# Kernel tuning notes

Measured on AMD Instinct MI355X. Metric: run time of the kernel, lower is better.

## Reference

```python
import jax, jax.numpy as jnp
import numpy as np
from jax import lax

B, T, D, H, L = 64, 1024, 256, 1024, 2


def setup_inputs() -> dict:
    key = jax.random.key(0)
    ks = jax.random.split(key, 9)
    s = 0.03  # small init so tanh/sigmoid stay in sane range
    return {
        "x": jax.random.normal(ks[0], (B, T, D), dtype=jnp.float32),
        "W_ih0": jax.random.normal(ks[1], (4 * H, D), dtype=jnp.float32) * s,
        "W_hh0": jax.random.normal(ks[2], (4 * H, H), dtype=jnp.float32) * s,
        "b_ih0": jax.random.normal(ks[3], (4 * H,), dtype=jnp.float32) * s,
        "b_hh0": jax.random.normal(ks[4], (4 * H,), dtype=jnp.float32) * s,
        "W_ih1": jax.random.normal(ks[5], (4 * H, H), dtype=jnp.float32) * s,
        "W_hh1": jax.random.normal(ks[6], (4 * H, H), dtype=jnp.float32) * s,
        "b_ih1": jax.random.normal(ks[7], (4 * H,), dtype=jnp.float32) * s,
        "b_hh1": jax.random.normal(ks[8], (4 * H,), dtype=jnp.float32) * s,
    }


def _lstm_layer(x, W_ih, W_hh, b_ih, b_hh):
    """Single LSTM layer over full sequence. x: [B,T,Din]. Returns (ys [B,T,H], h [B,H], c [B,H])."""
    b, t = x.shape[0], x.shape[1]
    h_dim = W_hh.shape[1]
    # Precompute input projections for all timesteps in one GEMM.
    xg = jnp.einsum('bti,gi->btg', x, W_ih) + b_ih + b_hh  # [B,T,4H]

    def step(carry, xg_t):
        h, c = carry
        g = xg_t + h @ W_hh.T  # [B,4H]
        i, f, gg, o = jnp.split(g, 4, axis=-1)  # PyTorch gate order i,f,g,o
        i = jax.nn.sigmoid(i)
        f = jax.nn.sigmoid(f)
        gg = jnp.tanh(gg)
        o = jax.nn.sigmoid(o)
        c = f * c + i * gg
        h = o * jnp.tanh(c)
        return (h, c), h

    h0 = jnp.zeros((b, h_dim), x.dtype)
    (h, c), ys = lax.scan(step, (h0, h0), jnp.swapaxes(xg, 0, 1))
    return jnp.swapaxes(ys, 0, 1), h, c


def reference(x, W_ih0, W_hh0, b_ih0, b_hh0, W_ih1, W_hh1, b_ih1, b_hh1):
    # Dropout layers are identity in eval mode; nn.LSTM inter-layer dropout
    # is also inactive in eval, so the math is a plain stacked LSTM whose
    # final (h, c) per layer is returned, matching the torch forward().
    y0, h0_, c0_ = _lstm_layer(x, W_ih0, W_hh0, b_ih0, b_hh0)
    _, h1_, c1_ = _lstm_layer(y0, W_ih1, W_hh1, b_ih1, b_hh1)
    h = jnp.stack([h0_, h1_], axis=0)  # [L,B,H]
    c = jnp.stack([c0_, c1_], axis=0)  # [L,B,H]
    return (h, c)
```

## Files before the change

kernel.cpp:

```cpp
#include <hip/hip_runtime.h>

#define NWG     256
#define TPB     256
#define NL0     128
#define T_STEPS 1024
#define HD      1024
#define DIN     256
#define K0      1280
#define K1      2048
#define K0P     1288
#define K1P     2056
#define SMEM_BYTES (32*K1P*2)

#define HSLAB_BYTES 131072ull
#define HSLAB_U64   16384
#define HIST_DEPTH  1025
#define HIST_BYTES  (HIST_DEPTH*HSLAB_BYTES)
#define X8_BYTES    33554432ull
#define FLAGS_BYTES 32768ull

typedef float  f32x4  __attribute__((ext_vector_type(4)));
typedef __bf16 bf16x8 __attribute__((ext_vector_type(8)));
typedef int    i32x4  __attribute__((ext_vector_type(4)));
typedef unsigned long long u64;

__device__ __forceinline__ unsigned short f2bf(float f){
  union { float f; unsigned u; } a; a.f = f;
  unsigned u = a.u;
  u += 0x7fffu + ((u >> 16) & 1u);
  return (unsigned short)(u >> 16);
}
__device__ __forceinline__ float sigmf(float x){ return 1.0f/(1.0f + __expf(-x)); }
__device__ __forceinline__ float tanhf_fast(float x){ return 2.0f*sigmf(2.0f*x) - 1.0f; }

__device__ __forceinline__ u64 ld64c(const u64* p){
  return __hip_atomic_load(p, __ATOMIC_RELAXED, __HIP_MEMORY_SCOPE_AGENT);
}
__device__ __forceinline__ unsigned ldflag(const unsigned* p){
  return __hip_atomic_load(p, __ATOMIC_RELAXED, __HIP_MEMORY_SCOPE_AGENT);
}
__device__ __forceinline__ void stflag(unsigned* p, unsigned v){
  __hip_atomic_store(p, v, __ATOMIC_RELAXED, __HIP_MEMORY_SCOPE_AGENT);
}
__device__ __forceinline__ void st128c(void* p, i32x4 v){
  asm volatile("global_store_dwordx4 %0, %1, off sc0 sc1" :: "v"(p), "v"(v) : "memory");
}

__global__ void xpose_kernel(const float* __restrict__ x, unsigned short* __restrict__ X8){
  int idx   = blockIdx.x*256 + threadIdx.x;
  int t     = idx >> 11;
  int rem   = idx & 2047;
  int plane = rem >> 6;
  int b     = rem & 63;
  const float* src = x + ((size_t)b << 18) + (t << 8) + (plane << 3);
  unsigned short tmp[8];
  #pragma unroll
  for (int j = 0; j < 8; ++j) tmp[j] = f2bf(src[j]);
  int4 v; __builtin_memcpy(&v, tmp, 16);
  ((int4*)X8)[idx] = v;
}

template<bool H0C, bool H1C>
__global__ void __launch_bounds__(TPB, 1)
lstm_mega(const float* __restrict__ Wih0, const float* __restrict__ Whh0,
          const float* __restrict__ bih0, const float* __restrict__ bhh0,
          const float* __restrict__ Wih1, const float* __restrict__ Whh1,
          const float* __restrict__ bih1, const float* __restrict__ bhh1,
          const unsigned short* __restrict__ X8,
          unsigned* flags, unsigned* gen,
          u64* H0, u64* H1, int d0, int d1,
          float* __restrict__ out)
{
  extern __shared__ unsigned short Ws[];
  const int tid   = threadIdx.x;
  const int wg    = blockIdx.x;
  const int layer = (wg >= NL0);
  const int wgl   = layer ? wg - NL0 : wg;
  const int KD    = layer ? K1  : K0;
  const int dlen  = layer ? HD  : DIN;
  const int KP    = layer ? K1P : K0P;
  const int4* X4  = (const int4*)X8;

  {
    const float* Wih = layer ? Wih1 : Wih0;
    const float* Whh = layer ? Whh1 : Whh0;
    for (int m = 0; m < 32; ++m){
      int gr = (m & 3)*HD + wgl*8 + (m >> 2);
      const float* ar = Wih + (size_t)gr*dlen;
      const float* br = Whh + (size_t)gr*HD;
      unsigned short* row = Ws + m*KP;
      for (int k = tid; k < KD; k += TPB)
        row[k] = f2bf(k < dlen ? ar[k] : br[k - dlen]);
    }
  }
  __syncthreads();

  const int lane  = tid & 63;
  const int wv    = tid >> 6;
  const int q     = lane >> 4;
  const int nn    = lane & 15;
  const int batch = wv*16 + nn;

  float bias[2][4];
  {
    const float* bi = layer ? bih1 : bih0;
    const float* bh = layer ? bhh1 : bhh0;
    #pragma unroll
    for (int rt = 0; rt < 2; ++rt){
      int colr = wgl*8 + rt*4 + q;
      #pragma unroll
      for (int r = 0; r < 4; ++r)
        bias[rt][r] = bi[r*HD + colr] + bh[r*HD + colr];
    }
  }

  float cst[2] = {0.f, 0.f};
  float hv[2]  = {0.f, 0.f};
  f32x4 a00, a01, a10, a11;

  auto MM = [&](int kb, bf16x8 b){
    bf16x8 a0, a1;
    __builtin_memcpy(&a0, &Ws[nn*KP + kb*32 + q*8], 16);
    __builtin_memcpy(&a1, &Ws[(16+nn)*KP + kb*32 + q*8], 16);
    if (kb & 1){ a01 = __builtin_amdgcn_mfma_f32_16x16x32_bf16(a0,b,a01,0,0,0);
                 a11 = __builtin_amdgcn_mfma_f32_16x16x32_bf16(a1,b,a11,0,0,0); }
    else       { a00 = __builtin_amdgcn_mfma_f32_16x16x32_bf16(a0,b,a00,0,0,0);
                 a10 = __builtin_amdgcn_mfma_f32_16x16x32_bf16(a1,b,a10,0,0,0); }
  };
  auto CHUNK = [&](int kb0, u64* d){
    #pragma unroll
    for (int i = 0; i < 8; ++i){
      u64 pair[2] = {d[2*i], d[2*i+1]};
      bf16x8 b; __builtin_memcpy(&b, pair, 16);
      MM(kb0 + i, b);
    }
  };

  unsigned seenA = 0, seenB = 0;
  auto waitL0 = [&](unsigned ep){
    if (tid < NL0 && seenA < ep){
      const unsigned* p = &flags[tid*16];
      unsigned v = ldflag(p);
      while (v < ep){ __builtin_amdgcn_s_sleep(1); v = ldflag(p); }
      seenA = v;
    }
    __syncthreads();
  };
  auto waitL1 = [&](unsigned ep){
    if (tid < NL0 && seenB < ep){
      const unsigned* p = &flags[(NL0 + tid)*16];
      unsigned v = ldflag(p);
      while (v < ep){ __builtin_amdgcn_s_sleep(1); v = ldflag(p); }
      seenB = v;
    }
    __syncthreads();
  };
  auto postF = [&](unsigned ep){
    asm volatile("s_waitcnt vmcnt(0)" ::: "memory");
    __syncthreads();
    if (tid == 0) stflag(&flags[wg*16], ep);
  };
  auto waitAll = [&](unsigned ep){
    while (ldflag(&flags[tid*16]) < ep) __builtin_amdgcn_s_sleep(1);
    __syncthreads();
  };

  u64 B0[16], B1[16], B2[16];

  auto epilogue = [&](u64* Hw, int wd, int t){
    f32x4 s0 = a00 + a01, s1 = a10 + a11;
    #pragma unroll
    for (int rt = 0; rt < 2; ++rt){
      f32x4 s = rt ? s1 : s0;
      float ii = sigmf(s[0] + bias[rt][0]);
      float ff = sigmf(s[1] + bias[rt][1]);
      float gg = tanhf_fast(s[2] + bias[rt][2]);
      float oo = sigmf(s[3] + bias[rt][3]);
      cst[rt] = ff*cst[rt] + ii*gg;
      hv[rt]  = oo*tanhf_fast(cst[rt]);
    }
    unsigned hpk = ((unsigned)f2bf(hv[1]) << 16) | (unsigned)f2bf(hv[0]);
    unsigned g0 = __shfl(hpk, nn);
    unsigned g1 = __shfl(hpk, nn + 16);
    unsigned g2 = __shfl(hpk, nn + 32);
    unsigned g3 = __shfl(hpk, nn + 48);
    if (q == 0){
      i32x4 v;
      v.x = (int)((g0 & 0xffffu) | (g1 << 16));
      v.y = (int)((g2 & 0xffffu) | (g3 << 16));
      v.z = (int)((g0 >> 16) | (g1 & 0xffff0000u));
      v.w = (int)((g2 >> 16) | (g3 & 0xffff0000u));
      char* wbase = (char*)(Hw + (size_t)((t+1) % wd)*HSLAB_U64);
      st128c(wbase + ((wgl*64 + wv*16 + nn) << 4), v);
    }
  };

  auto step0 = [&](int t, bool dec){
    a00 = (f32x4){0,0,0,0}; a01 = a00; a10 = a00; a11 = a00;
    const int4* xb = X4 + (size_t)t*2048;
    const u64* hb  = H0 + (size_t)(t % d0)*HSLAB_U64;
    auto LDH = [&](int c, u64* d){
      #pragma unroll
      for (int i = 0; i < 8; ++i){
        const u64* p = hb + (((c*8 + i)*4 + q)*64 + batch)*2;
        d[2*i]   = H0C ? ld64c(p)     : p[0];
        d[2*i+1] = H0C ? ld64c(p + 1) : p[1];
      }
    };
    int4 xr[8];
    #pragma unroll
    for (int kb = 0; kb < 8; ++kb)
      xr[kb] = xb[(kb*4 + q)*64 + batch];
    #pragma unroll
    for (int kb = 0; kb < 6; ++kb){
      bf16x8 b; __builtin_memcpy(&b, &xr[kb], 16); MM(kb, b);
    }
    if (dec) waitL0((unsigned)t);
    LDH(0, B0); LDH(1, B1); LDH(2, B2);
    { bf16x8 b; __builtin_memcpy(&b, &xr[6], 16); MM(6, b);
                __builtin_memcpy(&b, &xr[7], 16); MM(7, b); }
    CHUNK(8,  B0); LDH(3, B0);
    CHUNK(16, B1);
    CHUNK(24, B2);
    CHUNK(32, B0);
    epilogue(H0, d0, t);
  };

  auto step1 = [&](int t, bool dec){
    a00 = (f32x4){0,0,0,0}; a01 = a00; a10 = a00; a11 = a00;
    const u64* yb = H0 + (size_t)((t+1) % d0)*HSLAB_U64;
    const u64* hb = H1 + (size_t)(t % d1)*HSLAB_U64;
    auto LDY = [&](int c, u64* d){
      #pragma unroll
      for (int i = 0; i < 8; ++i){
        const u64* p = yb + (((c*8 + i)*4 + q)*64 + batch)*2;
        d[2*i]   = H0C ? ld64c(p)     : p[0];
        d[2*i+1] = H0C ? ld64c(p + 1) : p[1];
      }
    };
    auto LDH = [&](int c, u64* d){
      #pragma unroll
      for (int i = 0; i < 8; ++i){
        const u64* p = hb + (((c*8 + i)*4 + q)*64 + batch)*2;
        d[2*i]   = H1C ? ld64c(p)     : p[0];
        d[2*i+1] = H1C ? ld64c(p + 1) : p[1];
      }
    };
    if (dec) waitL0((unsigned)(t+1));
    LDY(0, B0); LDY(1, B1); LDY(2, B2);
    CHUNK(0,  B0); LDY(3, B0);
    CHUNK(8,  B1);
    CHUNK(16, B2);
    if (dec) waitL1((unsigned)t);
    LDH(0, B1); LDH(1, B2);
    CHUNK(24, B0);
    LDH(2, B0);
    CHUNK(32, B1);
    LDH(3, B1);
    CHUNK(40, B2);
    CHUNK(48, B0);
    CHUNK(56, B1);
    epilogue(H1, d1, t);
  };

  const bool dec = (d0 >= T_STEPS + 1);
  if (!layer){
    if (dec){
      for (int s = 0; s < T_STEPS; ++s){ step0(s, true); postF((unsigned)(s+1)); }
    } else {
      for (int s = 0; s < T_STEPS; ++s){
        step0(s, false); postF((unsigned)(s+1)); waitAll((unsigned)(s+1));
      }
    }
  } else {
    if (dec){
      for (int t = 0; t < T_STEPS; ++t){ step1(t, true); postF((unsigned)(t+1)); }
    } else {
      for (int s = 0; s < T_STEPS; ++s){
        if (s > 0) step1(s-1, false);
        postF((unsigned)(s+1)); waitAll((unsigned)(s+1));
      }
      step1(T_STEPS-1, false);
    }
  }

  {
    int col0 = wgl*8 + q;
    int base = layer ? 65536 : 0;
    out[base          + batch*HD + col0    ] = hv[0];
    out[base          + batch*HD + col0 + 4] = hv[1];
    out[base + 131072 + batch*HD + col0    ] = cst[0];
    out[base + 131072 + batch*HD + col0 + 4] = cst[1];
  }
}

extern "C" void kernel_launch(void* const* d_in, const int* in_sizes, int n_in,
                              void* d_out, int out_size, void* d_ws, size_t ws_size,
                              hipStream_t stream)
{
  const float* x    = (const float*)d_in[0];
  const float* Wih0 = (const float*)d_in[1];
  const float* Whh0 = (const float*)d_in[2];
  const float* bih0 = (const float*)d_in[3];
  const float* bhh0 = (const float*)d_in[4];
  const float* Wih1 = (const float*)d_in[5];
  const float* Whh1 = (const float*)d_in[6];
  const float* bih1 = (const float*)d_in[7];
  const float* bhh1 = (const float*)d_in[8];
  float* out = (float*)d_out;

  char* ws = (char*)d_ws;
  unsigned* flags = (unsigned*)ws;
  unsigned* gen   = (unsigned*)(ws + 16384);

  const size_t need2 = FLAGS_BYTES + 2*HIST_BYTES + X8_BYTES;
  const size_t need1 = FLAGS_BYTES + HIST_BYTES + 2*HSLAB_BYTES + X8_BYTES;

  u64 *H0p, *H1p; unsigned short* X8p; int d0, d1, tier;
  if (ws_size >= need2){
    tier = 2; d0 = HIST_DEPTH; d1 = HIST_DEPTH;
    H0p = (u64*)(ws + FLAGS_BYTES);
    H1p = (u64*)(ws + FLAGS_BYTES + HIST_BYTES);
    X8p = (unsigned short*)(ws + FLAGS_BYTES + 2*HIST_BYTES);
  } else if (ws_size >= need1){
    tier = 1; d0 = HIST_DEPTH; d1 = 2;
    H0p = (u64*)(ws + FLAGS_BYTES);
    H1p = (u64*)(ws + FLAGS_BYTES + HIST_BYTES);
    X8p = (unsigned short*)(ws + FLAGS_BYTES + HIST_BYTES + 2*HSLAB_BYTES);
  } else {
    tier = 0; d0 = 2; d1 = 2;
    H0p = (u64*)(ws + FLAGS_BYTES);
    H1p = (u64*)(ws + FLAGS_BYTES + 2*HSLAB_BYTES);
    X8p = (unsigned short*)(ws + FLAGS_BYTES + 4*HSLAB_BYTES);
  }

  hipMemsetAsync(flags, 0, FLAGS_BYTES, stream);
  hipMemsetAsync(H0p, 0, HSLAB_BYTES, stream);
  hipMemsetAsync(H1p, 0, HSLAB_BYTES, stream);
  xpose_kernel<<<8192, 256, 0, stream>>>(x, X8p);

  void* fn = (tier == 2) ? (void*)&lstm_mega<false,false>
           : (tier == 1) ? (void*)&lstm_mega<false,true>
                         : (void*)&lstm_mega<true,true>;
  hipFuncSetAttribute(fn, hipFuncAttributeMaxDynamicSharedMemorySize, SMEM_BYTES);

  const unsigned short* X8c = X8p;
  void* args[] = {(void*)&Wih0,(void*)&Whh0,(void*)&bih0,(void*)&bhh0,
                  (void*)&Wih1,(void*)&Whh1,(void*)&bih1,(void*)&bhh1,
                  (void*)&X8c,(void*)&flags,(void*)&gen,
                  (void*)&H0p,(void*)&H1p,(void*)&d0,(void*)&d1,(void*)&out};
  hipError_t err = hipLaunchCooperativeKernel(fn, dim3(NWG), dim3(TPB),
                                              args, SMEM_BYTES, stream);
  if (err != hipSuccess){
    if (tier == 2)
      lstm_mega<false,false><<<dim3(NWG), dim3(TPB), SMEM_BYTES, stream>>>(
        Wih0,Whh0,bih0,bhh0,Wih1,Whh1,bih1,bhh1,X8c,flags,gen,H0p,H1p,d0,d1,out);
    else if (tier == 1)
      lstm_mega<false,true><<<dim3(NWG), dim3(TPB), SMEM_BYTES, stream>>>(
        Wih0,Whh0,bih0,bhh0,Wih1,Whh1,bih1,bhh1,X8c,flags,gen,H0p,H1p,d0,d1,out);
    else
      lstm_mega<true,true><<<dim3(NWG), dim3(TPB), SMEM_BYTES, stream>>>(
        Wih0,Whh0,bih0,bhh0,Wih1,Whh1,bih1,bhh1,X8c,flags,gen,H0p,H1p,d0,d1,out);
  }
}
```

Baseline: 5.933 ms.

## Switch LSTM recurrence to 32x32x16 MFMA with split-K across waves

Each step's gate GEMM now uses 32x32x16 bf16 MFMA instead of 16x16x32. The K dimension is split across the four waves, each covering 32 rows by 64 batches, and partial sums are reduced through an LDS scratch buffer with extra barriers. Weight rows in LDS drop the padding and use an XOR swizzle to avoid bank conflicts. The hidden state is packed through LDS before a single coalesced store. The aim is fewer MFMA instructions and fewer redundant A-operand loads per step, at the cost of an LDS reduction and two added __syncthreads per step.

```diff
diff --git a/kernel.cpp b/kernel.cpp
--- a/kernel.cpp
+++ b/kernel.cpp
@@ -8,9 +8,11 @@
 #define DIN     256
 #define K0      1280
 #define K1      2048
-#define K0P     1288
-#define K1P     2056
-#define SMEM_BYTES (32*K1P*2)
+
+#define SCR_OFF   (32*K1*2)
+#define SCR_BYTES (4*3*64*8*4)
+#define PACK_OFF  (SCR_OFF + SCR_BYTES)
+#define SMEM_BYTES (PACK_OFF + 64*16)
 
 #define HSLAB_BYTES 131072ull
 #define HSLAB_U64   16384
@@ -20,6 +22,7 @@
 #define FLAGS_BYTES 32768ull
 
 typedef float  f32x4  __attribute__((ext_vector_type(4)));
+typedef float  f32x16 __attribute__((ext_vector_type(16)));
 typedef __bf16 bf16x8 __attribute__((ext_vector_type(8)));
 typedef int    i32x4  __attribute__((ext_vector_type(4)));
 typedef unsigned long long u64;
@@ -71,15 +74,18 @@
           u64* H0, u64* H1, int d0, int d1,
           float* __restrict__ out)
 {
-  extern __shared__ unsigned short Ws[];
+  extern __shared__ char smem[];
+  unsigned short* Ws = (unsigned short*)smem;
+  float*          Sc = (float*)(smem + SCR_OFF);
+  unsigned short* Pk = (unsigned short*)(smem + PACK_OFF);
+
   const int tid   = threadIdx.x;
   const int wg    = blockIdx.x;
   const int layer = (wg >= NL0);
   const int wgl   = layer ? wg - NL0 : wg;
   const int KD    = layer ? K1  : K0;
   const int dlen  = layer ? HD  : DIN;
-  const int KP    = layer ? K1P : K0P;
-  const int4* X4  = (const int4*)X8;
+  const char* X8b = (const char*)X8;
 
   {
     const float* Wih = layer ? Wih1 : Wih0;
@@ -88,51 +94,66 @@
       int gr = (m & 3)*HD + wgl*8 + (m >> 2);
       const float* ar = Wih + (size_t)gr*dlen;
       const float* br = Whh + (size_t)gr*HD;
-      unsigned short* row = Ws + m*KP;
+      unsigned short* row = Ws + m*KD;
+      const int sw = (m & 7) << 3;
       for (int k = tid; k < KD; k += TPB)
-        row[k] = f2bf(k < dlen ? ar[k] : br[k - dlen]);
+        row[k ^ sw] = f2bf(k < dlen ? ar[k] : br[k - dlen]);
     }
   }
   __syncthreads();
 
   const int lane  = tid & 63;
   const int wv    = tid >> 6;
-  const int q     = lane >> 4;
-  const int nn    = lane & 15;
-  const int batch = wv*16 + nn;
-
-  float bias[2][4];
+  const int hi    = lane >> 5;
+  const int ln31  = lane & 31;
+  const unsigned short* Arow = Ws + ln31*KD;
+  const int axor  = (lane & 7) << 3;
+
+  const int rbo  = wv & 1;
+  const int bat  = (wv >> 1)*32 + ln31;
+  const int c0   = 4*rbo + hi;
+  const int c1   = c0 + 2;
+
+  float bias8[8];
   {
     const float* bi = layer ? bih1 : bih0;
     const float* bh = layer ? bhh1 : bhh0;
     #pragma unroll
-    for (int rt = 0; rt < 2; ++rt){
-      int colr = wgl*8 + rt*4 + q;
-      #pragma unroll
-      for (int r = 0; r < 4; ++r)
-        bias[rt][r] = bi[r*HD + colr] + bh[r*HD + colr];
+    for (int g = 0; g < 4; ++g){
+      bias8[g]     = bi[g*HD + wgl*8 + c0] + bh[g*HD + wgl*8 + c0];
+      bias8[4 + g] = bi[g*HD + wgl*8 + c1] + bh[g*HD + wgl*8 + c1];
     }
   }
 
   float cst[2] = {0.f, 0.f};
   float hv[2]  = {0.f, 0.f};
-  f32x4 a00, a01, a10, a11;
-
-  auto MM = [&](int kb, bf16x8 b){
-    bf16x8 a0, a1;
-    __builtin_memcpy(&a0, &Ws[nn*KP + kb*32 + q*8], 16);
-    __builtin_memcpy(&a1, &Ws[(16+nn)*KP + kb*32 + q*8], 16);
-    if (kb & 1){ a01 = __builtin_amdgcn_mfma_f32_16x16x32_bf16(a0,b,a01,0,0,0);
-                 a11 = __builtin_amdgcn_mfma_f32_16x16x32_bf16(a1,b,a11,0,0,0); }
-    else       { a00 = __builtin_amdgcn_mfma_f32_16x16x32_bf16(a0,b,a00,0,0,0);
-                 a10 = __builtin_amdgcn_mfma_f32_16x16x32_bf16(a1,b,a10,0,0,0); }
-  };
-  auto CHUNK = [&](int kb0, u64* d){
-    #pragma unroll
-    for (int i = 0; i < 8; ++i){
-      u64 pair[2] = {d[2*i], d[2*i+1]};
-      bf16x8 b; __builtin_memcpy(&b, pair, 16);
-      MM(kb0 + i, b);
+  f32x16 acc0, acc1;
+
+  auto LDC = [&](const char* slab, int j0, int sOff, bool coh, u64* d){
+    #pragma unroll
+    for (int jj = 0; jj < 4; ++jj){
+      const int sp = 4*(j0 + jj) + wv - sOff;
+      const char* p0 = slab + (((2*sp + hi)*64 + ln31) << 4);
+      const u64* pa = (const u64*)p0;
+      const u64* pb = (const u64*)(p0 + 512);
+      d[4*jj+0] = coh ? ld64c(pa)     : pa[0];
+      d[4*jj+1] = coh ? ld64c(pa + 1) : pa[1];
+      d[4*jj+2] = coh ? ld64c(pb)     : pb[0];
+      d[4*jj+3] = coh ? ld64c(pb + 1) : pb[1];
+    }
+  };
+  auto CHUNK = [&](int j0, u64* d){
+    #pragma unroll
+    for (int jj = 0; jj < 4; ++jj){
+      const int s = 4*(j0 + jj) + wv;
+      bf16x8 a, b0, b1;
+      __builtin_memcpy(&a, Arow + ((16*s + 8*hi) ^ axor), 16);
+      u64 q0[2] = {d[4*jj+0], d[4*jj+1]};
+      u64 q1[2] = {d[4*jj+2], d[4*jj+3]};
+      __builtin_memcpy(&b0, q0, 16);
+      __builtin_memcpy(&b1, q1, 16);
+      acc0 = __builtin_amdgcn_mfma_f32_32x32x16_bf16(a, b0, acc0, 0, 0, 0);
+      acc1 = __builtin_amdgcn_mfma_f32_32x32x16_bf16(a, b1, acc1, 0, 0, 0);
     }
   };
 
@@ -168,98 +189,98 @@
   u64 B0[16], B1[16], B2[16];
 
   auto epilogue = [&](u64* Hw, int wd, int t){
-    f32x4 s0 = a00 + a01, s1 = a10 + a11;
-    #pragma unroll
-    for (int rt = 0; rt < 2; ++rt){
-      f32x4 s = rt ? s1 : s0;
-      float ii = sigmf(s[0] + bias[rt][0]);
-      float ff = sigmf(s[1] + bias[rt][1]);
-      float gg = tanhf_fast(s[2] + bias[rt][2]);
-      float oo = sigmf(s[3] + bias[rt][3]);
-      cst[rt] = ff*cst[rt] + ii*gg;
-      hv[rt]  = oo*tanhf_fast(cst[rt]);
-    }
-    unsigned hpk = ((unsigned)f2bf(hv[1]) << 16) | (unsigned)f2bf(hv[0]);
-    unsigned g0 = __shfl(hpk, nn);
-    unsigned g1 = __shfl(hpk, nn + 16);
-    unsigned g2 = __shfl(hpk, nn + 32);
-    unsigned g3 = __shfl(hpk, nn + 48);
-    if (q == 0){
-      i32x4 v;
-      v.x = (int)((g0 & 0xffffu) | (g1 << 16));
-      v.y = (int)((g2 & 0xffffu) | (g3 << 16));
-      v.z = (int)((g0 >> 16) | (g1 & 0xffff0000u));
-      v.w = (int)((g2 >> 16) | (g3 & 0xffff0000u));
+    #pragma unroll
+    for (int dst = 0; dst < 4; ++dst){
+      if (dst == wv) continue;
+      const int slot = (wv - dst - 1) & 3;
+      const int rb   = dst & 1;
+      const f32x16 S = (dst & 2) ? acc1 : acc0;
+      f32x4 lo = { S[8*rb+0], S[8*rb+1], S[8*rb+2], S[8*rb+3] };
+      f32x4 hb = { S[8*rb+4], S[8*rb+5], S[8*rb+6], S[8*rb+7] };
+      float* q = Sc + ((dst*3 + slot)*64 + lane)*8;
+      *(f32x4*)(q)     = lo;
+      *(f32x4*)(q + 4) = hb;
+    }
+    __syncthreads();
+    f32x4 vlo, vhi;
+    if      (wv == 0){ vlo = (f32x4){acc0[0],acc0[1],acc0[2],acc0[3]};
+                       vhi = (f32x4){acc0[4],acc0[5],acc0[6],acc0[7]}; }
+    else if (wv == 1){ vlo = (f32x4){acc0[8],acc0[9],acc0[10],acc0[11]};
+                       vhi = (f32x4){acc0[12],acc0[13],acc0[14],acc0[15]}; }
+    else if (wv == 2){ vlo = (f32x4){acc1[0],acc1[1],acc1[2],acc1[3]};
+                       vhi = (f32x4){acc1[4],acc1[5],acc1[6],acc1[7]}; }
+    else             { vlo = (f32x4){acc1[8],acc1[9],acc1[10],acc1[11]};
+                       vhi = (f32x4){acc1[12],acc1[13],acc1[14],acc1[15]}; }
+    #pragma unroll
+    for (int ss = 0; ss < 3; ++ss){
+      const float* q = Sc + ((wv*3 + ss)*64 + lane)*8;
+      vlo += *(const f32x4*)(q);
+      vhi += *(const f32x4*)(q + 4);
+    }
+    {
+      float ii = sigmf(vlo[0] + bias8[0]);
+      float ff = sigmf(vlo[1] + bias8[1]);
+      float gg = tanhf_fast(vlo[2] + bias8[2]);
+      float oo = sigmf(vlo[3] + bias8[3]);
+      cst[0] = ff*cst[0] + ii*gg;
+      hv[0]  = oo*tanhf_fast(cst[0]);
+      ii = sigmf(vhi[0] + bias8[4]);
+      ff = sigmf(vhi[1] + bias8[5]);
+      gg = tanhf_fast(vhi[2] + bias8[6]);
+      oo = sigmf(vhi[3] + bias8[7]);
+      cst[1] = ff*cst[1] + ii*gg;
+      hv[1]  = oo*tanhf_fast(cst[1]);
+    }
+    Pk[bat*8 + c0] = f2bf(hv[0]);
+    Pk[bat*8 + c1] = f2bf(hv[1]);
+    __syncthreads();
+    if (tid < 64){
+      i32x4 v; __builtin_memcpy(&v, Pk + tid*8, 16);
       char* wbase = (char*)(Hw + (size_t)((t+1) % wd)*HSLAB_U64);
-      st128c(wbase + ((wgl*64 + wv*16 + nn) << 4), v);
+      st128c(wbase + ((wgl*64 + tid) << 4), v);
     }
   };
 
   auto step0 = [&](int t, bool dec){
-    a00 = (f32x4){0,0,0,0}; a01 = a00; a10 = a00; a11 = a00;
-    const int4* xb = X4 + (size_t)t*2048;
-    const u64* hb  = H0 + (size_t)(t % d0)*HSLAB_U64;
-    auto LDH = [&](int c, u64* d){
-      #pragma unroll
-      for (int i = 0; i < 8; ++i){
-        const u64* p = hb + (((c*8 + i)*4 + q)*64 + batch)*2;
-        d[2*i]   = H0C ? ld64c(p)     : p[0];
-        d[2*i+1] = H0C ? ld64c(p + 1) : p[1];
-      }
-    };
-    int4 xr[8];
-    #pragma unroll
-    for (int kb = 0; kb < 8; ++kb)
-      xr[kb] = xb[(kb*4 + q)*64 + batch];
-    #pragma unroll
-    for (int kb = 0; kb < 6; ++kb){
-      bf16x8 b; __builtin_memcpy(&b, &xr[kb], 16); MM(kb, b);
-    }
+    acc0 = (f32x16)(0.f); acc1 = (f32x16)(0.f);
+    const char* xb = X8b + ((size_t)t << 15);
+    const char* hb = (const char*)(H0 + (size_t)(t % d0)*HSLAB_U64);
+    LDC(xb, 0, 0, false, B0);
     if (dec) waitL0((unsigned)t);
-    LDH(0, B0); LDH(1, B1); LDH(2, B2);
-    { bf16x8 b; __builtin_memcpy(&b, &xr[6], 16); MM(6, b);
-                __builtin_memcpy(&b, &xr[7], 16); MM(7, b); }
-    CHUNK(8,  B0); LDH(3, B0);
+    LDC(hb, 4, 16, H0C, B1);
+    LDC(hb, 8, 16, H0C, B2);
+    CHUNK(0, B0);
+    LDC(hb, 12, 16, H0C, B0);
+    CHUNK(4, B1);
+    LDC(hb, 16, 16, H0C, B1);
+    CHUNK(8, B2);
+    CHUNK(12, B0);
     CHUNK(16, B1);
-    CHUNK(24, B2);
-    CHUNK(32, B0);
     epilogue(H0, d0, t);
   };
 
   auto step1 = [&](int t, bool dec){
-    a00 = (f32x4){0,0,0,0}; a01 = a00; a10 = a00; a11 = a00;
-    const u64* yb = H0 + (size_t)((t+1) % d0)*HSLAB_U64;
-    const u64* hb = H1 + (size_t)(t % d1)*HSLAB_U64;
-    auto LDY = [&](int c, u64* d){
-      #pragma unroll
-      for (int i = 0; i < 8; ++i){
-        const u64* p = yb + (((c*8 + i)*4 + q)*64 + batch)*2;
-        d[2*i]   = H0C ? ld64c(p)     : p[0];
-        d[2*i+1] = H0C ? ld64c(p + 1) : p[1];
-      }
-    };
-    auto LDH = [&](int c, u64* d){
-      #pragma unroll
-      for (int i = 0; i < 8; ++i){
-        const u64* p = hb + (((c*8 + i)*4 + q)*64 + batch)*2;
-        d[2*i]   = H1C ? ld64c(p)     : p[0];
-        d[2*i+1] = H1C ? ld64c(p + 1) : p[1];
-      }
-    };
+    acc0 = (f32x16)(0.f); acc1 = (f32x16)(0.f);
+    const char* yb = (const char*)(H0 + (size_t)((t+1) % d0)*HSLAB_U64);
+    const char* hb = (const char*)(H1 + (size_t)(t % d1)*HSLAB_U64);
     if (dec) waitL0((unsigned)(t+1));
-    LDY(0, B0); LDY(1, B1); LDY(2, B2);
-    CHUNK(0,  B0); LDY(3, B0);
-    CHUNK(8,  B1);
-    CHUNK(16, B2);
+    LDC(yb, 0, 0, H0C, B0);
+    LDC(yb, 4, 0, H0C, B1);
+    LDC(yb, 8, 0, H0C, B2);
+    CHUNK(0, B0);
+    LDC(yb, 12, 0, H0C, B0);
+    CHUNK(4, B1);
+    CHUNK(8, B2);
     if (dec) waitL1((unsigned)t);
-    LDH(0, B1); LDH(1, B2);
+    LDC(hb, 16, 64, H1C, B1);
+    LDC(hb, 20, 64, H1C, B2);
+    CHUNK(12, B0);
+    LDC(hb, 24, 64, H1C, B0);
+    CHUNK(16, B1);
+    LDC(hb, 28, 64, H1C, B1);
+    CHUNK(20, B2);
     CHUNK(24, B0);
-    LDH(2, B0);
-    CHUNK(32, B1);
-    LDH(3, B1);
-    CHUNK(40, B2);
-    CHUNK(48, B0);
-    CHUNK(56, B1);
+    CHUNK(28, B1);
     epilogue(H1, d1, t);
   };
 
@@ -285,12 +306,11 @@
   }
 
   {
-    int col0 = wgl*8 + q;
-    int base = layer ? 65536 : 0;
-    out[base          + batch*HD + col0    ] = hv[0];
-    out[base          + batch*HD + col0 + 4] = hv[1];
-    out[base + 131072 + batch*HD + col0    ] = cst[0];
-    out[base + 131072 + batch*HD + col0 + 4] = cst[1];
+    const int base = layer ? 65536 : 0;
+    out[base          + bat*HD + wgl*8 + c0] = hv[0];
+    out[base          + bat*HD + wgl*8 + c1] = hv[1];
+    out[base + 131072 + bat*HD + wgl*8 + c0] = cst[0];
+    out[base + 131072 + bat*HD + wgl*8 + c1] = cst[1];
   }
 }
 
```

New measurement: 6.846 ms. 15.4% more time.

## Repartition MFMA work so each wave owns one weight row-group and two batch tiles

Applied to the files above, without the earlier changes.

Each wave used to compute both 16-row weight tiles for its own 16 batches, loading two A fragments per k-block and keeping four accumulators. Now waves split by row-group and batch half: each wave loads one A fragment from shared memory and reuses it across two batch tiles. This halves LDS weight traffic per MFMA and doubles reuse of global h loads across the two accumulators. The h-slab stores become two 8-byte coherent stores, and the tier-2 path that kept a full layer-1 history is removed, so layer 1 always uses a 2-deep ring with coherent loads.

```diff
diff --git a/kernel.cpp b/kernel.cpp
--- a/kernel.cpp
+++ b/kernel.cpp
@@ -21,6 +21,7 @@
 
 typedef float  f32x4  __attribute__((ext_vector_type(4)));
 typedef __bf16 bf16x8 __attribute__((ext_vector_type(8)));
+typedef int    i32x2  __attribute__((ext_vector_type(2)));
 typedef int    i32x4  __attribute__((ext_vector_type(4)));
 typedef unsigned long long u64;
 
@@ -42,8 +43,8 @@
 __device__ __forceinline__ void stflag(unsigned* p, unsigned v){
   __hip_atomic_store(p, v, __ATOMIC_RELAXED, __HIP_MEMORY_SCOPE_AGENT);
 }
-__device__ __forceinline__ void st128c(void* p, i32x4 v){
-  asm volatile("global_store_dwordx4 %0, %1, off sc0 sc1" :: "v"(p), "v"(v) : "memory");
+__device__ __forceinline__ void st64c(void* p, i32x2 v){
+  asm volatile("global_store_dwordx2 %0, %1, off sc0 sc1" :: "v"(p), "v"(v) : "memory");
 }
 
 __global__ void xpose_kernel(const float* __restrict__ x, unsigned short* __restrict__ X8){
@@ -79,7 +80,7 @@
   const int KD    = layer ? K1  : K0;
   const int dlen  = layer ? HD  : DIN;
   const int KP    = layer ? K1P : K0P;
-  const int4* X4  = (const int4*)X8;
+  const char* X8b = (const char*)X8;
 
   {
     const float* Wih = layer ? Wih1 : Wih0;
@@ -95,44 +96,53 @@
   }
   __syncthreads();
 
-  const int lane  = tid & 63;
-  const int wv    = tid >> 6;
-  const int q     = lane >> 4;
-  const int nn    = lane & 15;
-  const int batch = wv*16 + nn;
-
-  float bias[2][4];
+  const int lane = tid & 63;
+  const int wv   = tid >> 6;
+  const int q    = lane >> 4;
+  const int nn   = lane & 15;
+  const int rg   = wv & 1;
+  const int bh   = wv >> 1;
+  const int bat0 = bh*32 + nn;
+  const int arow = rg*16 + nn;
+  const int c    = rg*4 + q;
+
+  float bias4[4];
   {
     const float* bi = layer ? bih1 : bih0;
-    const float* bh = layer ? bhh1 : bhh0;
+    const float* bp = layer ? bhh1 : bhh0;
     #pragma unroll
-    for (int rt = 0; rt < 2; ++rt){
-      int colr = wgl*8 + rt*4 + q;
-      #pragma unroll
-      for (int r = 0; r < 4; ++r)
-        bias[rt][r] = bi[r*HD + colr] + bh[r*HD + colr];
-    }
+    for (int g = 0; g < 4; ++g)
+      bias4[g] = bi[g*HD + wgl*8 + c] + bp[g*HD + wgl*8 + c];
   }
 
   float cst[2] = {0.f, 0.f};
   float hv[2]  = {0.f, 0.f};
-  f32x4 a00, a01, a10, a11;
-
-  auto MM = [&](int kb, bf16x8 b){
-    bf16x8 a0, a1;
-    __builtin_memcpy(&a0, &Ws[nn*KP + kb*32 + q*8], 16);
-    __builtin_memcpy(&a1, &Ws[(16+nn)*KP + kb*32 + q*8], 16);
-    if (kb & 1){ a01 = __builtin_amdgcn_mfma_f32_16x16x32_bf16(a0,b,a01,0,0,0);
-                 a11 = __builtin_amdgcn_mfma_f32_16x16x32_bf16(a1,b,a11,0,0,0); }
-    else       { a00 = __builtin_amdgcn_mfma_f32_16x16x32_bf16(a0,b,a00,0,0,0);
-                 a10 = __builtin_amdgcn_mfma_f32_16x16x32_bf16(a1,b,a10,0,0,0); }
-  };
-  auto CHUNK = [&](int kb0, u64* d){
+  f32x4 acc0, acc1;
+
+  auto LD = [&](const char* slab, int kbl, bool coh, u64* d){
     #pragma unroll
-    for (int i = 0; i < 8; ++i){
-      u64 pair[2] = {d[2*i], d[2*i+1]};
-      bf16x8 b; __builtin_memcpy(&b, pair, 16);
-      MM(kb0 + i, b);
+    for (int jj = 0; jj < 4; ++jj){
+      const char* p = slab + ((((kbl + jj)*4 + q)*64 + bat0) << 4);
+      if (coh){
+        d[4*jj+0] = ld64c((const u64*)p);
+        d[4*jj+1] = ld64c((const u64*)p + 1);
+        d[4*jj+2] = ld64c((const u64*)(p + 256));
+        d[4*jj+3] = ld64c((const u64*)(p + 256) + 1);
+      } else {
+        __builtin_memcpy(&d[4*jj],   p,       16);
+        __builtin_memcpy(&d[4*jj+2], p + 256, 16);
+      }
+    }
+  };
+  auto CH = [&](int kb0, u64* d){
+    #pragma unroll
+    for (int jj = 0; jj < 4; ++jj){
+      bf16x8 a, b0, b1;
+      __builtin_memcpy(&a, &Ws[arow*KP + (kb0 + jj)*32 + q*8], 16);
+      __builtin_memcpy(&b0, &d[4*jj],   16);
+      __builtin_memcpy(&b1, &d[4*jj+2], 16);
+      acc0 = __builtin_amdgcn_mfma_f32_16x16x32_bf16(a, b0, acc0, 0, 0, 0);
+      acc1 = __builtin_amdgcn_mfma_f32_16x16x32_bf16(a, b1, acc1, 0, 0, 0);
     }
   };
 
@@ -168,16 +178,19 @@
   u64 B0[16], B1[16], B2[16];
 
   auto epilogue = [&](u64* Hw, int wd, int t){
-    f32x4 s0 = a00 + a01, s1 = a10 + a11;
-    #pragma unroll
-    for (int rt = 0; rt < 2; ++rt){
-      f32x4 s = rt ? s1 : s0;
-      float ii = sigmf(s[0] + bias[rt][0]);
-      float ff = sigmf(s[1] + bias[rt][1]);
-      float gg = tanhf_fast(s[2] + bias[rt][2]);
-      float oo = sigmf(s[3] + bias[rt][3]);
-      cst[rt] = ff*cst[rt] + ii*gg;
-      hv[rt]  = oo*tanhf_fast(cst[rt]);
+    {
+      float ii = sigmf(acc0[0] + bias4[0]);
+      float ff = sigmf(acc0[1] + bias4[1]);
+      float gg = tanhf_fast(acc0[2] + bias4[2]);
+      float oo = sigmf(acc0[3] + bias4[3]);
+      cst[0] = ff*cst[0] + ii*gg;
+      hv[0]  = oo*tanhf_fast(cst[0]);
+      ii = sigmf(acc1[0] + bias4[0]);
+      ff = sigmf(acc1[1] + bias4[1]);
+      gg = tanhf_fast(acc1[2] + bias4[2]);
+      oo = sigmf(acc1[3] + bias4[3]);
+      cst[1] = ff*cst[1] + ii*gg;
+      hv[1]  = oo*tanhf_fast(cst[1]);
     }
     unsigned hpk = ((unsigned)f2bf(hv[1]) << 16) | (unsigned)f2bf(hv[0]);
     unsigned g0 = __shfl(hpk, nn);
@@ -185,81 +198,64 @@
     unsigned g2 = __shfl(hpk, nn + 32);
     unsigned g3 = __shfl(hpk, nn + 48);
     if (q == 0){
-      i32x4 v;
-      v.x = (int)((g0 & 0xffffu) | (g1 << 16));
-      v.y = (int)((g2 & 0xffffu) | (g3 << 16));
-      v.z = (int)((g0 >> 16) | (g1 & 0xffff0000u));
-      v.w = (int)((g2 >> 16) | (g3 & 0xffff0000u));
+      i32x2 v0, v1;
+      v0.x = (int)((g0 & 0xffffu) | (g1 << 16));
+      v0.y = (int)((g2 & 0xffffu) | (g3 << 16));
+      v1.x = (int)((g0 >> 16) | (g1 & 0xffff0000u));
+      v1.y = (int)((g2 >> 16) | (g3 & 0xffff0000u));
       char* wbase = (char*)(Hw + (size_t)((t+1) % wd)*HSLAB_U64);
-      st128c(wbase + ((wgl*64 + wv*16 + nn) << 4), v);
+      st64c(wbase + ((wgl*64 + bat0     ) << 4) + rg*8, v0);
+      st64c(wbase + ((wgl*64 + bat0 + 16) << 4) + rg*8, v1);
     }
   };
 
   auto step0 = [&](int t, bool dec){
-    a00 = (f32x4){0,0,0,0}; a01 = a00; a10 = a00; a11 = a00;
-    const int4* xb = X4 + (size_t)t*2048;
-    const u64* hb  = H0 + (size_t)(t % d0)*HSLAB_U64;
-    auto LDH = [&](int c, u64* d){
-      #pragma unroll
-      for (int i = 0; i < 8; ++i){
-        const u64* p = hb + (((c*8 + i)*4 + q)*64 + batch)*2;
-        d[2*i]   = H0C ? ld64c(p)     : p[0];
-        d[2*i+1] = H0C ? ld64c(p + 1) : p[1];
-      }
-    };
-    int4 xr[8];
-    #pragma unroll
-    for (int kb = 0; kb < 8; ++kb)
-      xr[kb] = xb[(kb*4 + q)*64 + batch];
-    #pragma unroll
-    for (int kb = 0; kb < 6; ++kb){
-      bf16x8 b; __builtin_memcpy(&b, &xr[kb], 16); MM(kb, b);
-    }
+    acc0 = (f32x4){0,0,0,0}; acc1 = acc0;
+    const char* xb = X8b + ((size_t)t << 15);
+    const char* hb = (const char*)(H0 + (size_t)(t % d0)*HSLAB_U64);
+    LD(xb, 0, false, B0);
+    LD(xb, 4, false, B1);
     if (dec) waitL0((unsigned)t);
-    LDH(0, B0); LDH(1, B1); LDH(2, B2);
-    { bf16x8 b; __builtin_memcpy(&b, &xr[6], 16); MM(6, b);
-                __builtin_memcpy(&b, &xr[7], 16); MM(7, b); }
-    CHUNK(8,  B0); LDH(3, B0);
-    CHUNK(16, B1);
-    CHUNK(24, B2);
-    CHUNK(32, B0);
+    LD(hb, 0,  H0C, B2);
+    CH(0,  B0); LD(hb, 4,  H0C, B0);
+    CH(4,  B1); LD(hb, 8,  H0C, B1);
+    CH(8,  B2); LD(hb, 12, H0C, B2);
+    CH(12, B0); LD(hb, 16, H0C, B0);
+    CH(16, B1); LD(hb, 20, H0C, B1);
+    CH(20, B2); LD(hb, 24, H0C, B2);
+    CH(24, B0); LD(hb, 28, H0C, B0);
+    CH(28, B1);
+    CH(32, B2);
+    CH(36, B0);
     epilogue(H0, d0, t);
   };
 
   auto step1 = [&](int t, bool dec){
-    a00 = (f32x4){0,0,0,0}; a01 = a00; a10 = a00; a11 = a00;
-    const u64* yb = H0 + (size_t)((t+1) % d0)*HSLAB_U64;
-    const u64* hb = H1 + (size_t)(t % d1)*HSLAB_U64;
-    auto LDY = [&](int c, u64* d){
-      #pragma unroll
-      for (int i = 0; i < 8; ++i){
-        const u64* p = yb + (((c*8 + i)*4 + q)*64 + batch)*2;
-        d[2*i]   = H0C ? ld64c(p)     : p[0];
-        d[2*i+1] = H0C ? ld64c(p + 1) : p[1];
-      }
-    };
-    auto LDH = [&](int c, u64* d){
-      #pragma unroll
-      for (int i = 0; i < 8; ++i){
-        const u64* p = hb + (((c*8 + i)*4 + q)*64 + batch)*2;
-        d[2*i]   = H1C ? ld64c(p)     : p[0];
-        d[2*i+1] = H1C ? ld64c(p + 1) : p[1];
-      }
-    };
+    acc0 = (f32x4){0,0,0,0}; acc1 = acc0;
+    const char* yb  = (const char*)(H0 + (size_t)((t+1) % d0)*HSLAB_U64);
+    const char* hb1 = (const char*)(H1 + (size_t)(t % d1)*HSLAB_U64);
     if (dec) waitL0((unsigned)(t+1));
-    LDY(0, B0); LDY(1, B1); LDY(2, B2);
-    CHUNK(0,  B0); LDY(3, B0);
-    CHUNK(8,  B1);
-    CHUNK(16, B2);
+    LD(yb, 0, H0C, B0);
+    LD(yb, 4, H0C, B1);
+    LD(yb, 8, H0C, B2);
+    CH(0,  B0); LD(yb, 12, H0C, B0);
+    CH(4,  B1); LD(yb, 16, H0C, B1);
+    CH(8,  B2); LD(yb, 20, H0C, B2);
+    CH(12, B0); LD(yb, 24, H0C, B0);
+    CH(16, B1); LD(yb, 28, H0C, B1);
+    CH(20, B2);
     if (dec) waitL1((unsigned)t);
-    LDH(0, B1); LDH(1, B2);
-    CHUNK(24, B0);
-    LDH(2, B0);
-    CHUNK(32, B1);
-    LDH(3, B1);
-    CHUNK(40, B2);
-    CHUNK(48, B0);
-    CHUNK(56, B1);
+    LD(hb1, 0, H1C, B2);
+    CH(24, B0); LD(hb1, 4,  H1C, B0);
+    CH(28, B1); LD(hb1, 8,  H1C, B1);
+    CH(32, B2); LD(hb1, 12, H1C, B2);
+    CH(36, B0); LD(hb1, 16, H1C, B0);
+    CH(40, B1); LD(hb1, 20, H1C, B1);
+    CH(44, B2); LD(hb1, 24, H1C, B2);
+    CH(48, B0); LD(hb1, 28, H1C, B0);
+    CH(52, B1);
+    CH(56, B2);
+    CH(60, B0);
     epilogue(H1, d1, t);
   };
 
@@ -285,12 +281,12 @@
   }
 
   {
-    int col0 = wgl*8 + q;
-    int base = layer ? 65536 : 0;
-    out[base          + batch*HD + col0    ] = hv[0];
-    out[base          + batch*HD + col0 + 4] = hv[1];
-    out[base + 131072 + batch*HD + col0    ] = cst[0];
-    out[base + 131072 + batch*HD + col0 + 4] = cst[1];
+    const int col = wgl*8 + c;
+    const int base = layer ? 65536 : 0;
+    out[base          + bat0*HD        + col] = hv[0];
+    out[base          + (bat0+16)*HD   + col] = hv[1];
+    out[base + 131072 + bat0*HD        + col] = cst[0];
+    out[base + 131072 + (bat0+16)*HD   + col] = cst[1];
   }
 }
 
@@ -313,16 +309,10 @@
   unsigned* flags = (unsigned*)ws;
   unsigned* gen   = (unsigned*)(ws + 16384);
 
-  const size_t need2 = FLAGS_BYTES + 2*HIST_BYTES + X8_BYTES;
-  const size_t need1 = FLAGS_BYTES + HIST_BYTES + 2*HSLAB_BYTES + X8_BYTES;
+  const size_t need_main = FLAGS_BYTES + HIST_BYTES + 2*HSLAB_BYTES + X8_BYTES;
 
   u64 *H0p, *H1p; unsigned short* X8p; int d0, d1, tier;
-  if (ws_size >= need2){
-    tier = 2; d0 = HIST_DEPTH; d1 = HIST_DEPTH;
-    H0p = (u64*)(ws + FLAGS_BYTES);
-    H1p = (u64*)(ws + FLAGS_BYTES + HIST_BYTES);
-    X8p = (unsigned short*)(ws + FLAGS_BYTES + 2*HIST_BYTES);
-  } else if (ws_size >= need1){
+  if (ws_size >= need_main){
     tier = 1; d0 = HIST_DEPTH; d1 = 2;
     H0p = (u64*)(ws + FLAGS_BYTES);
     H1p = (u64*)(ws + FLAGS_BYTES + HIST_BYTES);
@@ -339,8 +329,7 @@
   hipMemsetAsync(H1p, 0, HSLAB_BYTES, stream);
   xpose_kernel<<<8192, 256, 0, stream>>>(x, X8p);
 
-  void* fn = (tier == 2) ? (void*)&lstm_mega<false,false>
-           : (tier == 1) ? (void*)&lstm_mega<false,true>
+  void* fn = (tier == 1) ? (void*)&lstm_mega<false,true>
                          : (void*)&lstm_mega<true,true>;
   hipFuncSetAttribute(fn, hipFuncAttributeMaxDynamicSharedMemorySize, SMEM_BYTES);
 
@@ -352,10 +341,7 @@
   hipError_t err = hipLaunchCooperativeKernel(fn, dim3(NWG), dim3(TPB),
                                               args, SMEM_BYTES, stream);
   if (err != hipSuccess){
-    if (tier == 2)
-      lstm_mega<false,false><<<dim3(NWG), dim3(TPB), SMEM_BYTES, stream>>>(
-        Wih0,Whh0,bih0,bhh0,Wih1,Whh1,bih1,bhh1,X8c,flags,gen,H0p,H1p,d0,d1,out);
-    else if (tier == 1)
+    if (tier == 1)
       lstm_mega<false,true><<<dim3(NWG), dim3(TPB), SMEM_BYTES, stream>>>(
         Wih0,Whh0,bih0,bhh0,Wih1,Whh1,bih1,bhh1,X8c,flags,gen,H0p,H1p,d0,d1,out);
     else
```

After: 8.149 ms. +37.3%, slower.
